# Kernel optimization log

Measured on AMD Instinct MI355X. Metric: run time of the kernel, lower is better.

The kernel has to match this reference:

```python
import jax, jax.numpy as jnp
import numpy as np

B, F, H, W = 1, 6, 20, 26
S = F * H * W            # 3120 tokens
DIM, NH, HD = 1536, 12, 128
C = HD // 2              # 64 rotary channels
T_C = C - 2 * (C // 3)   # 22 temporal channels
H_C = C // 3             # 21
W_C = C // 3             # 21
LOCAL_FRAMES = 4         # local_attn_size (in frames)
SINK_FRAMES = 1          # sink_size (in frames)
EPS = 1e-6
MAX_POS = 1024


def _angle_table(n_ch):
    inv = 1.0 / (10000.0 ** (np.arange(n_ch, dtype=np.float64) / n_ch))
    return np.outer(np.arange(MAX_POS, dtype=np.float64), inv)


def setup_inputs() -> dict:
    key = jax.random.key(0)
    ks = jax.random.split(key, 8)
    sc = 0.02
    ang = np.concatenate([_angle_table(T_C), _angle_table(H_C), _angle_table(W_C)], axis=1)  # [1024, 64]
    return {
        "x": jax.random.normal(ks[0], (B, S, DIM), jnp.float32),
        "seq_lens": jnp.array([S], jnp.int32),
        "grid_sizes": jnp.array([[F, H, W]], jnp.int32),
        "freqs_cos": jnp.asarray(np.cos(ang), jnp.float32),
        "freqs_sin": jnp.asarray(np.sin(ang), jnp.float32),
        "Wq": jax.random.normal(ks[1], (DIM, DIM), jnp.float32) * sc,
        "bq": jnp.zeros((DIM,), jnp.float32),
        "Wk": jax.random.normal(ks[2], (DIM, DIM), jnp.float32) * sc,
        "bk": jnp.zeros((DIM,), jnp.float32),
        "Wv": jax.random.normal(ks[3], (DIM, DIM), jnp.float32) * sc,
        "bv": jnp.zeros((DIM,), jnp.float32),
        "Wo": jax.random.normal(ks[4], (DIM, DIM), jnp.float32) * sc,
        "bo": jnp.zeros((DIM,), jnp.float32),
        "gq": jnp.ones((DIM,), jnp.float32),
        "gk": jnp.ones((DIM,), jnp.float32),
    }


def _rms_norm(x, g):
    # WanRMSNorm: x * rsqrt(mean(x^2) + eps) * weight
    return x * jax.lax.rsqrt(jnp.mean(x * x, axis=-1, keepdims=True) + EPS) * g


def _rope_apply(x, freqs_cos, freqs_sin):
    # x: [B, S, NH, HD]; per-token 3D (f,h,w) rotary on consecutive pairs.
    pos = jnp.arange(S)
    f = pos // (H * W)
    hh = (pos // W) % H
    ww = pos % W
    cos_t, cos_h, cos_w = freqs_cos[:, :T_C], freqs_cos[:, T_C:T_C + H_C], freqs_cos[:, T_C + H_C:]
    sin_t, sin_h, sin_w = freqs_sin[:, :T_C], freqs_sin[:, T_C:T_C + H_C], freqs_sin[:, T_C + H_C:]
    cos = jnp.concatenate([cos_t[f], cos_h[hh], cos_w[ww]], axis=-1)[None, :, None, :]  # [1,S,1,C]
    sin = jnp.concatenate([sin_t[f], sin_h[hh], sin_w[ww]], axis=-1)[None, :, None, :]
    xp = x.reshape(B, S, NH, C, 2)
    xr, xi = xp[..., 0], xp[..., 1]
    out = jnp.stack([xr * cos - xi * sin, xr * sin + xi * cos], axis=-1)
    return out.reshape(B, S, NH, HD)


def _block_mask():
    # frame-causal + local window (in frames) + sink frames: [S, S] bool
    fid = jnp.arange(S) // (H * W)
    fi, fj = fid[:, None], fid[None, :]
    return (fj <= fi) & ((fi - fj < LOCAL_FRAMES) | (fj < SINK_FRAMES))


def reference(x, seq_lens, grid_sizes, freqs_cos, freqs_sin,
              Wq, bq, Wk, bk, Wv, bv, Wo, bo, gq, gk):
    q = _rms_norm(x @ Wq + bq, gq).reshape(B, S, NH, HD)
    k = _rms_norm(x @ Wk + bk, gk).reshape(B, S, NH, HD)
    v = (x @ Wv + bv).reshape(B, S, NH, HD)
    rq = _rope_apply(q, freqs_cos, freqs_sin)
    rk = _rope_apply(k, freqs_cos, freqs_sin)
    scale = 1.0 / jnp.sqrt(jnp.asarray(HD, x.dtype))
    scores = jnp.einsum('bind,bjnd->bnij', rq, rk) * scale  # [B,NH,S,S]
    scores = jnp.where(_block_mask()[None, None], scores, jnp.finfo(scores.dtype).min)
    attn = jax.nn.softmax(scores, axis=-1)
    out = jnp.einsum('bnij,bjnd->bind', attn, v).reshape(B, S, DIM)
    return out @ Wo + bo
```

## Files before the change

kernel.cpp:

```cpp
#include <hip/hip_runtime.h>
#include <hip/hip_bf16.h>
#include <stdint.h>

typedef short v8s __attribute__((ext_vector_type(8)));
typedef short v4h __attribute__((ext_vector_type(4)));
typedef float v4f __attribute__((ext_vector_type(4)));
typedef unsigned short u16;

#define S_LEN 3120
#define DIMN 1536
#define NHEAD 12
#define HDIM 128
#define FRM 520
#define NT64 49
#define T64_PH 166
#define TOT64 1992
#define NSTEP32 17
#define SCALE_QK 0.088388347648318447f
#define MAXOFF2 17.312340490667560f

struct TaskMap {
  unsigned char tile[T64_PH];
  unsigned char frame[T64_PH];
  short accv[NT64];
  unsigned char nf[NT64];
};
constexpr TaskMap make_map() {
  TaskMap m{};
  int acc = 0;
  for (int tile = 0; tile < NT64; ++tile) {
    int q0t = tile * 64;
    int f_lo = q0t / FRM;
    int qhi = q0t + 63 < S_LEN - 1 ? q0t + 63 : S_LEN - 1;
    int f_hi = qhi / FRM;
    int fstart = f_lo - 3 > 0 ? f_lo - 3 : 0;
    int sink = fstart > 0 ? 1 : 0;
    int nf = f_hi - fstart + 1 + sink;
    m.accv[tile] = (short)acc;
    m.nf[tile] = (unsigned char)nf;
    for (int c = 0; c < nf; ++c) {
      m.tile[acc + c] = (unsigned char)tile;
      m.frame[acc + c] = (unsigned char)(sink ? (c == 0 ? 0 : fstart + c - 1) : (fstart + c));
    }
    acc += nf;
  }
  return m;
}
__device__ __constant__ TaskMap TM = make_map();

__device__ __forceinline__ v4f mfma16(v8s a, v8s b, v4f c) {
  return __builtin_amdgcn_mfma_f32_16x16x32_bf16(a, b, c, 0, 0, 0);
}
__device__ __forceinline__ float b2f(u16 u) {
  union { float f; unsigned int i; } x; x.i = ((unsigned int)u) << 16; return x.f;
}
__device__ __forceinline__ u16 f2b(float f) {
  union { float f; unsigned int i; } x; x.f = f;
  unsigned int r = x.i + 0x7FFFu + ((x.i >> 16) & 1u);
  return (u16)(r >> 16);
}
__device__ __forceinline__ void async16(const void* g, void* l) {
  __builtin_amdgcn_global_load_lds(
      (__attribute__((address_space(1))) const void*)g,
      (__attribute__((address_space(3))) void*)l, 16, 0, 0);
}
__device__ __forceinline__ int xcd_chunk(int o, int nwg) {
  int q = nwg >> 3, r = nwg & 7;
  int xcd = o & 7, idx = o >> 3;
  return (xcd < r ? xcd * (q + 1) : r * (q + 1) + (xcd - r) * q) + idx;
}
__device__ __forceinline__ int wave_isf(const u16* __restrict__ w) {
  int l = threadIdx.x & 63;
  u16 m0 = (u16)(w[2 * l] & 0x7FFF);
  u16 m1 = (u16)(w[2 * l + 1] & 0x7FFF);
  return __ballot(m0 >= 0x4480 || m1 >= 0x4480) != 0ull;
}

struct PrepArgs {
  const void* tin[4]; u16* tout[4];
  const void* csrc[9]; u16* cdst[9]; int cn[9];
};
__global__ __launch_bounds__(256) void prep(PrepArgs a, const u16* __restrict__ wsniff) {
  int isf = wave_isf(wsniff);
  int z = blockIdx.z;
  int t = threadIdx.x;
  int bidx = blockIdx.y * gridDim.x + blockIdx.x;
  if (z < 4) {
    __shared__ u16 tile[32][33];
    const float* inf = (const float*)a.tin[z];
    const u16* inb = (const u16*)a.tin[z];
    u16* out = a.tout[z];
    int tx = t & 31, ty = t >> 5;
    int gr0 = blockIdx.y * 32, gc0 = blockIdx.x * 32;
#pragma unroll
    for (int i = 0; i < 4; ++i) {
      int r = ty + i * 8;
      size_t idx = (size_t)(gr0 + r) * DIMN + gc0 + tx;
      tile[r][tx] = isf ? f2b(inf[idx]) : inb[idx];
    }
    __syncthreads();
#pragma unroll
    for (int i = 0; i < 4; ++i) {
      int r = ty + i * 8;
      out[(size_t)(gc0 + r) * DIMN + gr0 + tx] = tile[tx][r];
    }
  } else {
    int id = z - 4;
    int n4 = a.cn[id] >> 2;
    const float* sf = (const float*)a.csrc[id];
    const u16* sb = (const u16*)a.csrc[id];
    u16* d = a.cdst[id];
    int stride = gridDim.x * gridDim.y * 256;
    for (int i = bidx * 256 + t; i < n4; i += stride) {
      v4h o;
      if (isf) {
        float4 x4 = *(const float4*)(sf + (size_t)i * 4);
        o[0] = (short)f2b(x4.x); o[1] = (short)f2b(x4.y);
        o[2] = (short)f2b(x4.z); o[3] = (short)f2b(x4.w);
      } else {
        o = *(const v4h*)(sb + (size_t)i * 4);
      }
      *(v4h*)(d + (size_t)i * 4) = o;
    }
  }
}

template <int MT, int NT>
__global__ __launch_bounds__(256) void gemm3(
    const u16* __restrict__ A,
    const u16* BT0, const u16* BT1, const u16* BT2,
    const u16* b0, const u16* b1, const u16* b2,
    void* C0, void* C1, void* C2, int M, const u16* __restrict__ wsniff, int dyn) {
  static_assert(MT == 64, "4-wave layout assumes MT==64");
  int nwg = 588 * gridDim.z;
  int o = blockIdx.x + 12 * blockIdx.y + 588 * blockIdx.z;
  int s = xcd_chunk(o, nwg);
  int bx = s % 12, by = (s / 12) % 49, bz = s / 588;
  const u16* BT; const u16* bias; void* C;
  if (bz == 0)      { BT = BT0; bias = b0; C = C0; }
  else if (bz == 1) { BT = BT1; bias = b1; C = C1; }
  else              { BT = BT2; bias = b2; C = C2; }
  int f32out = dyn ? wave_isf(wsniff) : 0;
  __shared__ __align__(16) short As[MT * 64];
  __shared__ __align__(16) short Bs[NT * 64];
  int t = threadIdx.x, w = t >> 6, l = t & 63;
  int ln = l & 15, lg = l >> 4;
  int m0 = by * MT, n0 = bx * NT;
  int lr = l >> 3;
  int gl = (l & 7) ^ lr;
  constexpr int ACH = MT / 32;
  constexpr int BCH = NT / 32;
  const u16* gAp[ACH]; short* lAp[ACH];
#pragma unroll
  for (int i = 0; i < ACH; ++i) {
    int c = w * ACH + i;
    int arow = min(m0 + c * 8 + lr, M - 1);
    gAp[i] = A + (size_t)arow * DIMN + gl * 8;
    lAp[i] = As + c * 512;
  }
  const u16* gBp[BCH]; short* lBp[BCH];
#pragma unroll
  for (int i = 0; i < BCH; ++i) {
    int c = w * BCH + i;
    int brow = n0 + c * 8 + lr;
    gBp[i] = BT + (size_t)brow * DIMN + gl * 8;
    lBp[i] = Bs + c * 512;
  }
  constexpr int NJ = NT / 64;
  int aoff[2][4], boff[2][NJ];
#pragma unroll
  for (int ks = 0; ks < 2; ++ks) {
#pragma unroll
    for (int i = 0; i < 4; ++i) {
      int ar = i * 16 + ln;
      aoff[ks][i] = ar * 64 + (((ks * 4 + lg) ^ (ar & 7)) * 8);
    }
#pragma unroll
    for (int j = 0; j < NJ; ++j) {
      int br = w * (NJ * 16) + j * 16 + ln;
      boff[ks][j] = br * 64 + (((ks * 4 + lg) ^ (br & 7)) * 8);
    }
  }
  v4f acc[4][NJ] = {};
  for (int k0 = 0; k0 < DIMN; k0 += 64) {
    __syncthreads();
#pragma unroll
    for (int i = 0; i < ACH; ++i) async16(gAp[i] + k0, lAp[i]);
#pragma unroll
    for (int i = 0; i < BCH; ++i) async16(gBp[i] + k0, lBp[i]);
    __syncthreads();
#pragma unroll
    for (int ks = 0; ks < 2; ++ks) {
      v8s af[4], bfr[NJ];
#pragma unroll
      for (int i = 0; i < 4; ++i) af[i] = *(const v8s*)(As + aoff[ks][i]);
#pragma unroll
      for (int j = 0; j < NJ; ++j) bfr[j] = *(const v8s*)(Bs + boff[ks][j]);
#pragma unroll
      for (int i = 0; i < 4; ++i)
#pragma unroll
        for (int j = 0; j < NJ; ++j) acc[i][j] = mfma16(af[i], bfr[j], acc[i][j]);
    }
  }
  if ((!dyn) && bz == 2) {
#pragma unroll
    for (int i = 0; i < 4; ++i) {
      int rb = m0 + i * 16 + lg * 4;
      if (rb + 3 >= M) continue;
#pragma unroll
      for (int j = 0; j < NJ; ++j) {
        int col = n0 + w * (NJ * 16) + j * 16 + ln;
        float bv = b2f(bias[col]);
        v4h pk;
#pragma unroll
        for (int r = 0; r < 4; ++r) pk[r] = (short)f2b(acc[i][j][r] + bv);
        *(v4h*)((u16*)C + (size_t)col * S_LEN + rb) = pk;
      }
    }
    return;
  }
#pragma unroll
  for (int i = 0; i < 4; ++i) {
    int rb = m0 + i * 16 + lg * 4;
#pragma unroll
    for (int j = 0; j < NJ; ++j) {
      int col = n0 + w * (NJ * 16) + j * 16 + ln;
      float bv = b2f(bias[col]);
#pragma unroll
      for (int r = 0; r < 4; ++r) {
        int grow = rb + r;
        if (grow < M) {
          size_t idx = (size_t)grow * DIMN + col;
          float val = acc[i][j][r] + bv;
          if (f32out) ((float*)C)[idx] = val;
          else        ((u16*)C)[idx] = f2b(val);
        }
      }
    }
  }
}

__global__ __launch_bounds__(256) void norm_rope(u16* __restrict__ Q, u16* __restrict__ K,
                                                 const u16* __restrict__ gq,
                                                 const u16* __restrict__ gk,
                                                 const u16* __restrict__ fcos,
                                                 const u16* __restrict__ fsin) {
  int t = threadIdx.x, w = t >> 6, l = t & 63;
  int s = blockIdx.x * 4 + w;
  u16* base = (blockIdx.y == 0 ? Q : K) + (size_t)s * DIMN;
  const u16* g = (blockIdx.y == 0) ? gq : gk;
  v8s xv[3], gv[3];
#pragma unroll
  for (int c = 0; c < 3; ++c) {
    xv[c] = *(const v8s*)(base + c * 512 + l * 8);
    gv[c] = *(const v8s*)(g + c * 512 + l * 8);
  }
  float x[24];
  float ss = 0.f;
#pragma unroll
  for (int c = 0; c < 3; ++c)
#pragma unroll
    for (int j = 0; j < 8; ++j) {
      float v = b2f((u16)xv[c][j]);
      x[c * 8 + j] = v;
      ss += v * v;
    }
#pragma unroll
  for (int off = 32; off > 0; off >>= 1) ss += __shfl_xor(ss, off);
  float rs = rsqrtf(ss * (1.0f / DIMN) + 1e-6f);
  if (blockIdx.y == 0) rs *= SCALE_QK * 1.4426950408889634f;
  int f = s / FRM;
  int hh = (s / 26) % 20;
  int ww = s % 26;
#pragma unroll
  for (int c = 0; c < 3; ++c) {
    v8s out;
#pragma unroll
    for (int u = 0; u < 4; ++u) {
      int e0 = c * 512 + l * 8 + 2 * u;
      int ch = (e0 & 127) >> 1;
      int p = (ch < 22) ? f : ((ch < 43) ? hh : ww);
      float co = b2f(fcos[p * 64 + ch]);
      float si = b2f(fsin[p * 64 + ch]);
      float xr = x[c * 8 + 2 * u] * rs * b2f((u16)gv[c][2 * u]);
      float xi = x[c * 8 + 2 * u + 1] * rs * b2f((u16)gv[c][2 * u + 1]);
      out[2 * u]     = (short)f2b(xr * co - xi * si);
      out[2 * u + 1] = (short)f2b(xr * si + xi * co);
    }
    *(v8s*)(base + c * 512 + l * 8) = out;
  }
}

__global__ __launch_bounds__(256) void attn_block(const u16* __restrict__ Q,
                                                  const u16* __restrict__ K,
                                                  const u16* __restrict__ VT,
                                                  u16* __restrict__ Po,
                                                  float* __restrict__ Pl) {
  __shared__ __align__(16) short Ks[32 * 128];
  __shared__ __align__(16) short Vs[128 * 32];
  __shared__ __align__(16) short Pt[4][16 * 40];
  int t = threadIdx.x, w = t >> 6, l = t & 63;
  int ln = l & 15, lg = l >> 4;
  int o = blockIdx.x;
  int task = (o & 7) * 249 + (o >> 3);
  int head = task / T64_PH, tid = task % T64_PH;
  int tile = TM.tile[tid], frame = TM.frame[tid];
  int q0 = tile * 64 + w * 16;
  v8s qf[4];
  bool rowok[4];
  {
    int row = min(q0 + ln, S_LEN - 1);
    const u16* qp = Q + (size_t)row * DIMN + head * HDIM + lg * 8;
#pragma unroll
    for (int c = 0; c < 4; ++c) qf[c] = *(const v8s*)(qp + c * 32);
#pragma unroll
    for (int r = 0; r < 4; ++r) {
      int qr = q0 + lg * 4 + r;
      int fi = (qr < S_LEN) ? qr / FRM : -1;
      rowok[r] = (frame <= fi) && ((fi - frame) < 4 || frame == 0);
    }
  }
  float lsum[4] = {};
  v4f o_acc[8] = {};
  int kbeg = frame * FRM, kend = kbeg + FRM;
  int kr_i[2], kgl_i[2], vd_i[2], vgl_i[2];
#pragma unroll
  for (int i = 0; i < 2; ++i) {
    int n = (w * 2 + i) * 64 + l;
    kr_i[i] = n >> 4;
    kgl_i[i] = (n & 15) ^ (kr_i[i] & 15);
    vd_i[i] = n >> 2;
    vgl_i[i] = (n & 3) ^ (vd_i[i] & 3);
  }
  const u16* Kb = K + head * HDIM;
  for (int it = 0; it < NSTEP32; ++it) {
    int kb = kbeg + it * 32;
    __syncthreads();
#pragma unroll
    for (int i = 0; i < 2; ++i) {
      int krow = min(kb + kr_i[i], S_LEN - 1);
      async16(Kb + (size_t)krow * DIMN + kgl_i[i] * 8,
              (char*)Ks + (size_t)(w * 2 + i) * 1024);
      async16(VT + (size_t)(head * HDIM + vd_i[i]) * S_LEN + kb + vgl_i[i] * 8,
              (char*)Vs + (size_t)(w * 2 + i) * 1024);
    }
    __syncthreads();
    v4f s[2] = {};
    __builtin_amdgcn_s_setprio(1);
#pragma unroll
    for (int kg = 0; kg < 2; ++kg) {
#pragma unroll
      for (int c = 0; c < 4; ++c) {
        v8s kf = *(const v8s*)(&Ks[(kg * 16 + ln) * 128 + (((c * 4 + lg) ^ ln) * 8)]);
        s[kg] = mfma16(qf[c], kf, s[kg]);
      }
    }
    __builtin_amdgcn_s_setprio(0);
#pragma unroll
    for (int kg = 0; kg < 2; ++kg) {
      bool jv = (kb + kg * 16 + ln) < kend;
#pragma unroll
      for (int r = 0; r < 4; ++r) {
        float p = (rowok[r] && jv) ? exp2f(s[kg][r] - MAXOFF2) : 0.f;
        unsigned int bi = __float_as_uint(p) & 0xffff0000u;
        lsum[r] += __uint_as_float(bi);
        Pt[w][(lg * 4 + r) * 40 + kg * 16 + ln] = (u16)(bi >> 16);
      }
    }
    v8s pf0 = *(const v8s*)(&Pt[w][ln * 40 + lg * 8]);
    __builtin_amdgcn_s_setprio(1);
#pragma unroll
    for (int d = 0; d < 8; ++d) {
      int rr = d * 16 + ln;
      v8s vf = *(const v8s*)(&Vs[rr * 32 + ((lg ^ (rr & 3)) * 8)]);
      o_acc[d] = mfma16(pf0, vf, o_acc[d]);
    }
    __builtin_amdgcn_s_setprio(0);
  }
#pragma unroll
  for (int r = 0; r < 4; ++r) {
    float v = lsum[r];
    v += __shfl_xor(v, 1);
    v += __shfl_xor(v, 2);
    v += __shfl_xor(v, 4);
    v += __shfl_xor(v, 8);
    lsum[r] = v;
  }
  size_t pbase = (size_t)task * (64 * 128);
#pragma unroll
  for (int d = 0; d < 8; ++d)
#pragma unroll
    for (int r = 0; r < 4; ++r) {
      int lrow = w * 16 + lg * 4 + r;
      Po[pbase + lrow * 128 + d * 16 + ln] = f2b(o_acc[d][r]);
    }
  if (ln == 0) {
#pragma unroll
    for (int r = 0; r < 4; ++r)
      Pl[task * 64 + w * 16 + lg * 4 + r] = lsum[r];
  }
}

__global__ __launch_bounds__(256) void attn_combine(const u16* __restrict__ Po,
                                                    const float* __restrict__ Pl,
                                                    u16* __restrict__ Oa) {
  int tile = blockIdx.x, h = blockIdx.y;
  int accv = TM.accv[tile], nf = TM.nf[tile];
  int base = h * T64_PH + accv;
  int t = threadIdx.x;
  int row = t >> 2, seg = (t & 3) * 32;
  int grow = tile * 64 + row;
  if (grow >= S_LEN) return;
  float lsum = 0.f;
  float ao[32];
#pragma unroll
  for (int j = 0; j < 32; ++j) ao[j] = 0.f;
  for (int c = 0; c < nf; ++c) {
    int task = base + c;
    lsum += Pl[task * 64 + row];
    const u16* p = Po + (size_t)task * 8192 + row * 128 + seg;
#pragma unroll
    for (int v = 0; v < 4; ++v) {
      v8s x = *(const v8s*)(p + v * 8);
#pragma unroll
      for (int j = 0; j < 8; ++j) ao[v * 8 + j] += b2f((u16)x[j]);
    }
  }
  float inv = 1.0f / lsum;
  u16* dst = Oa + (size_t)grow * DIMN + h * HDIM + seg;
#pragma unroll
  for (int v = 0; v < 4; ++v) {
    v8s res;
#pragma unroll
    for (int j = 0; j < 8; ++j) res[j] = (short)f2b(ao[v * 8 + j] * inv);
    *(v8s*)(dst + v * 8) = res;
  }
}

extern "C" void kernel_launch(void* const* d_in, const int* in_sizes, int n_in,
                              void* d_out, int out_size, void* d_ws, size_t ws_size,
                              hipStream_t stream) {
  (void)n_in; (void)out_size; (void)ws_size;
  u16* ws = (u16*)d_ws;
  size_t off = 16;
  const size_t SD = (size_t)S_LEN * DIMN;
  const size_t WW = (size_t)DIMN * DIMN;
  const size_t NPO = (size_t)1032 * 128 * 128;
  auto alloc = [&](size_t n) { u16* p = ws + off; off += (n + 7) & ~(size_t)7; return p; };
  u16* Xc  = alloc(SD);
  u16* Fc  = alloc(65536);
  u16* Fs  = alloc(65536);
  u16* bqc = alloc(1536); u16* bkc = alloc(1536); u16* bvc = alloc(1536); u16* boc = alloc(1536);
  u16* gqc = alloc(1536); u16* gkc = alloc(1536);
  u16* Qr = alloc(SD); u16* Kr = alloc(SD);
  u16* VT = alloc(SD);
  u16* Oa = alloc(SD);
  u16* WoT = alloc(WW);
  u16* WqT = alloc(WW); u16* WkT = alloc(WW); u16* WvT = alloc(WW);
  alloc(NPO - 3 * WW);
  float* Pl = (float*)alloc((size_t)TOT64 * 64 * 2);
  u16* Po = WqT;
  const u16* wsniff = (const u16*)d_in[5];

  PrepArgs pa;
  pa.tin[0] = d_in[5];  pa.tout[0] = WqT;
  pa.tin[1] = d_in[7];  pa.tout[1] = WkT;
  pa.tin[2] = d_in[9];  pa.tout[2] = WvT;
  pa.tin[3] = d_in[11]; pa.tout[3] = WoT;
  const int srcIdx[9] = {0, 3, 4, 6, 8, 10, 12, 13, 14};
  u16* dsts[9] = {Xc, Fc, Fs, bqc, bkc, bvc, boc, gqc, gkc};
  for (int i = 0; i < 9; ++i) {
    pa.csrc[i] = d_in[srcIdx[i]];
    pa.cdst[i] = dsts[i];
    pa.cn[i] = in_sizes[srcIdx[i]];
  }
  dim3 b256(256);
  prep<<<dim3(48, 48, 13), b256, 0, stream>>>(pa, wsniff);
  gemm3<64, 128><<<dim3(12, 49, 3), b256, 0, stream>>>(Xc, WqT, WkT, WvT, bqc, bkc, bvc,
                                                       Qr, Kr, VT, S_LEN, wsniff, 0);
  norm_rope<<<dim3(S_LEN / 4, 2), b256, 0, stream>>>(Qr, Kr, gqc, gkc, Fc, Fs);
  attn_block<<<dim3(TOT64), dim3(256), 0, stream>>>(Qr, Kr, VT, Po, Pl);
  attn_combine<<<dim3(NT64, NHEAD), b256, 0, stream>>>(Po, Pl, Oa);
  gemm3<64, 128><<<dim3(12, 49, 1), b256, 0, stream>>>(Oa, WoT, WoT, WoT, boc, boc, boc,
                                                       d_out, d_out, d_out, S_LEN, wsniff, 1);
}
```

Baseline: 334.4 us.

## Pair attention tasks sharing a key frame into 512-thread blocks

Groups two 64-row query tiles that attend to the same key frame into one 512-thread workgroup, so each K/V chunk loaded into LDS is reused by eight waves instead of four. The per-thread async load count halves and the grid shrinks to pairs per head with an XCD-aware block mapping. Odd leftover tiles run with a dead half that still joins the barriers but masks its work and skips the store. This cuts global K/V traffic and load instructions, at the cost of larger blocks, possibly lower occupancy, and idle waves in unpaired blocks.

```diff
diff --git a/kernel.cpp b/kernel.cpp
--- a/kernel.cpp
+++ b/kernel.cpp
@@ -47,6 +47,30 @@
   return m;
 }
 __device__ __constant__ TaskMap TM = make_map();
+
+struct TaskMap2 {
+  unsigned char tidA[96];
+  unsigned char tidB[96];
+  int npair;
+};
+constexpr TaskMap2 make_map2() {
+  TaskMap2 m{};
+  TaskMap tm = make_map();
+  int np = 0;
+  for (int f = 0; f < 6; ++f) {
+    int last = -1;
+    for (int tid = 0; tid < T64_PH; ++tid) {
+      if (tm.frame[tid] != f) continue;
+      if (last < 0) last = tid;
+      else { m.tidA[np] = (unsigned char)last; m.tidB[np] = (unsigned char)tid; ++np; last = -1; }
+    }
+    if (last >= 0) { m.tidA[np] = (unsigned char)last; m.tidB[np] = 0xFF; ++np; }
+  }
+  m.npair = np;
+  return m;
+}
+__device__ __constant__ TaskMap2 TM2 = make_map2();
+constexpr int NPAIR2 = make_map2().npair;
 
 __device__ __forceinline__ v4f mfma16(v8s a, v8s b, v4f c) {
   return __builtin_amdgcn_mfma_f32_16x16x32_bf16(a, b, c, 0, 0, 0);
@@ -291,21 +315,25 @@
   }
 }
 
-__global__ __launch_bounds__(256) void attn_block(const u16* __restrict__ Q,
+__global__ __launch_bounds__(512) void attn_block(const u16* __restrict__ Q,
                                                   const u16* __restrict__ K,
                                                   const u16* __restrict__ VT,
                                                   u16* __restrict__ Po,
                                                   float* __restrict__ Pl) {
   __shared__ __align__(16) short Ks[32 * 128];
   __shared__ __align__(16) short Vs[128 * 32];
-  __shared__ __align__(16) short Pt[4][16 * 40];
+  __shared__ __align__(16) short Pt[8][16 * 40];
   int t = threadIdx.x, w = t >> 6, l = t & 63;
   int ln = l & 15, lg = l >> 4;
-  int o = blockIdx.x;
-  int task = (o & 7) * 249 + (o >> 3);
-  int head = task / T64_PH, tid = task % T64_PH;
+  int b = xcd_chunk(blockIdx.x, NPAIR2 * NHEAD);
+  int head = b / NPAIR2, pid = b % NPAIR2;
+  int sub = w >> 2, w4 = w & 3;
+  int tidX = sub ? TM2.tidB[pid] : TM2.tidA[pid];
+  bool live = (tidX != 0xFF);
+  int tid = live ? tidX : TM2.tidA[pid];
   int tile = TM.tile[tid], frame = TM.frame[tid];
-  int q0 = tile * 64 + w * 16;
+  int task = head * T64_PH + tid;
+  int q0 = tile * 64 + w4 * 16;
   v8s qf[4];
   bool rowok[4];
   {
@@ -317,32 +345,24 @@
     for (int r = 0; r < 4; ++r) {
       int qr = q0 + lg * 4 + r;
       int fi = (qr < S_LEN) ? qr / FRM : -1;
-      rowok[r] = (frame <= fi) && ((fi - frame) < 4 || frame == 0);
+      rowok[r] = live && (frame <= fi) && ((fi - frame) < 4 || frame == 0);
     }
   }
   float lsum[4] = {};
   v4f o_acc[8] = {};
   int kbeg = frame * FRM, kend = kbeg + FRM;
-  int kr_i[2], kgl_i[2], vd_i[2], vgl_i[2];
-#pragma unroll
-  for (int i = 0; i < 2; ++i) {
-    int n = (w * 2 + i) * 64 + l;
-    kr_i[i] = n >> 4;
-    kgl_i[i] = (n & 15) ^ (kr_i[i] & 15);
-    vd_i[i] = n >> 2;
-    vgl_i[i] = (n & 3) ^ (vd_i[i] & 3);
-  }
+  int nslot = w * 64 + l;
+  int kr = nslot >> 4, kgl = (nslot & 15) ^ (kr & 15);
+  int vd = nslot >> 2, vgl = (nslot & 3) ^ (vd & 3);
   const u16* Kb = K + head * HDIM;
   for (int it = 0; it < NSTEP32; ++it) {
     int kb = kbeg + it * 32;
     __syncthreads();
-#pragma unroll
-    for (int i = 0; i < 2; ++i) {
-      int krow = min(kb + kr_i[i], S_LEN - 1);
-      async16(Kb + (size_t)krow * DIMN + kgl_i[i] * 8,
-              (char*)Ks + (size_t)(w * 2 + i) * 1024);
-      async16(VT + (size_t)(head * HDIM + vd_i[i]) * S_LEN + kb + vgl_i[i] * 8,
-              (char*)Vs + (size_t)(w * 2 + i) * 1024);
+    {
+      int krow = min(kb + kr, S_LEN - 1);
+      async16(Kb + (size_t)krow * DIMN + kgl * 8, (char*)Ks + (size_t)w * 1024);
+      async16(VT + (size_t)(head * HDIM + vd) * S_LEN + kb + vgl * 8,
+              (char*)Vs + (size_t)w * 1024);
     }
     __syncthreads();
     v4f s[2] = {};
@@ -377,6 +397,7 @@
     }
     __builtin_amdgcn_s_setprio(0);
   }
+  if (!live) return;
 #pragma unroll
   for (int r = 0; r < 4; ++r) {
     float v = lsum[r];
@@ -391,13 +412,13 @@
   for (int d = 0; d < 8; ++d)
 #pragma unroll
     for (int r = 0; r < 4; ++r) {
-      int lrow = w * 16 + lg * 4 + r;
+      int lrow = w4 * 16 + lg * 4 + r;
       Po[pbase + lrow * 128 + d * 16 + ln] = f2b(o_acc[d][r]);
     }
   if (ln == 0) {
 #pragma unroll
     for (int r = 0; r < 4; ++r)
-      Pl[task * 64 + w * 16 + lg * 4 + r] = lsum[r];
+      Pl[task * 64 + w4 * 16 + lg * 4 + r] = lsum[r];
   }
 }
 
@@ -479,7 +500,7 @@
   gemm3<64, 128><<<dim3(12, 49, 3), b256, 0, stream>>>(Xc, WqT, WkT, WvT, bqc, bkc, bvc,
                                                        Qr, Kr, VT, S_LEN, wsniff, 0);
   norm_rope<<<dim3(S_LEN / 4, 2), b256, 0, stream>>>(Qr, Kr, gqc, gkc, Fc, Fs);
-  attn_block<<<dim3(TOT64), dim3(256), 0, stream>>>(Qr, Kr, VT, Po, Pl);
+  attn_block<<<dim3(NPAIR2 * NHEAD), dim3(512), 0, stream>>>(Qr, Kr, VT, Po, Pl);
   attn_combine<<<dim3(NT64, NHEAD), b256, 0, stream>>>(Po, Pl, Oa);
   gemm3<64, 128><<<dim3(12, 49, 1), b256, 0, stream>>>(Oa, WoT, WoT, WoT, boc, boc, boc,
                                                        d_out, d_out, d_out, S_LEN, wsniff, 1);
```

Result: slower. 351.9 us (+5.2%).
